# Kernel tuning notes

Hardware: AMD Instinct MI355X
Metric: run time of the kernel (lower is better)

## Reference

```python
import jax, jax.numpy as jnp
import numpy as np

B, D, OUT = 256, 63, 128
DP = D + 1  # 64


def setup_inputs() -> dict:
    key = jax.random.key(0)
    k1, k2, k3, k4, k5 = jax.random.split(key, 5)
    return {
        "x": jax.random.normal(k1, (B, D), dtype=jnp.float32),
        "protein_output": jax.random.normal(k2, (B, D), dtype=jnp.float32),
        "dynamic_output": jax.random.normal(k3, (B, D), dtype=jnp.float32),
        "W": jax.random.normal(k4, (DP ** 3, OUT), dtype=jnp.float32) * 0.02,
        "b": jax.random.normal(k5, (OUT,), dtype=jnp.float32) * 0.02,
    }


def reference(x, protein_output, dynamic_output, W, b):
    bsz = x.shape[0]
    ones = jnp.ones((bsz, 1), dtype=x.dtype)
    a = jnp.concatenate([x, ones], axis=1)               # [B, D+1]
    p = jnp.concatenate([protein_output, ones], axis=1)   # [B, D+1]
    d = jnp.concatenate([dynamic_output, ones], axis=1)   # [B, D+1]
    # rank-1 trilinear outer product, flattened row-major: idx = (i*(D+1)+j)*(D+1)+k
    ab = jnp.einsum('bi,bj->bij', a, p)                   # [B, D+1, D+1]
    abc = jnp.einsum('bij,bk->bijk', ab, d)               # [B, D+1, D+1, D+1]
    feat = abc.reshape(bsz, -1)                           # [B, (D+1)^3]
    return feat @ W + b                                   # [B, OUT]
```

## Files before the change

### kernel.cpp

```cpp
#include <hip/hip_runtime.h>
#include <hip/hip_bf16.h>

typedef __attribute__((ext_vector_type(8))) short short8v;
typedef __attribute__((ext_vector_type(4))) float floatx4;
typedef __attribute__((ext_vector_type(4))) unsigned int uint4v;

__device__ __forceinline__ unsigned int pkbf(float a, float b) {
  __hip_bfloat162 h = __float22bfloat162_rn(make_float2(a, b));
  union { __hip_bfloat162 h; unsigned int u; } c; c.h = h;
  return c.u;
}

__global__ void bias_init(const float* __restrict__ bias, float* __restrict__ out) {
  int idx = blockIdx.x * 256 + threadIdx.x;
  out[idx] = bias[idx & 127];
}

__global__ __launch_bounds__(512)
void reduce_v3(const float* __restrict__ part, const float* __restrict__ bias,
               float* __restrict__ out) {
  const int tid = threadIdx.x;
  const int o = tid & 127;
  const int qr = tid >> 7;
  const int og = blockIdx.x * 128 + o;

  const float* pp = part + (((long)(qr * 64)) << 15) + og;
  float s0 = 0.f, s1 = 0.f, s2 = 0.f, s3 = 0.f;
  #pragma unroll 4
  for (int n = 0; n < 64; n += 4) {
    s0 += __builtin_nontemporal_load(pp + ((long)n << 15));
    s1 += __builtin_nontemporal_load(pp + ((long)(n + 1) << 15));
    s2 += __builtin_nontemporal_load(pp + ((long)(n + 2) << 15));
    s3 += __builtin_nontemporal_load(pp + ((long)(n + 3) << 15));
  }
  float sum = (s0 + s1) + (s2 + s3);

  __shared__ float red[3][128];
  if (qr) red[qr - 1][o] = sum;
  __syncthreads();
  if (qr == 0)
    out[og] = sum + red[0][o] + red[1][o] + red[2][o] + bias[o];
}

__global__ __launch_bounds__(512, 2)
void tfn_gemm_v3(const float* __restrict__ X, const float* __restrict__ P,
                 const float* __restrict__ Dyn, const float* __restrict__ W,
                 float* __restrict__ part) {
  __shared__ __align__(16) float wt0[4160];
  __shared__ __align__(16) float wt1[4160];
  __shared__ float p_lds[16][256];

  const int tid = threadIdx.x;
  const int wv = tid >> 6, lane = tid & 63;
  const int q = lane >> 4, l16 = lane & 15;
  const int r = wv & 3;
  const int cg = wv >> 2;

  const int c = blockIdx.x;
  const int i = c >> 2;
  const int j0 = (c & 3) << 4;

  const uint4v* wsrc = (const uint4v*)(W + (((long)c) << 10) * 128);

  uint4v rg0 = __builtin_nontemporal_load(&wsrc[tid]);
  uint4v rg1 = __builtin_nontemporal_load(&wsrc[512 + tid]);

  for (int idx = tid; idx < 256 * 16; idx += 512) {
    int bb = idx >> 4, jj = idx & 15;
    int j = j0 + jj;
    p_lds[jj][bb] = (j < 63) ? P[bb * 63 + j] : 1.0f;
  }

  float e[4][2][8];
  #pragma unroll
  for (int rt = 0; rt < 4; ++rt) {
    int brow = (r << 6) + (rt << 4) + l16;
    float av = (i < 63) ? X[brow * 63 + i] : 1.0f;
    #pragma unroll
    for (int h = 0; h < 2; ++h) {
      int kb = (h << 5) + (q << 3);
      #pragma unroll
      for (int t = 0; t < 8; ++t) {
        int k = kb + t;
        float dv = (k < 63) ? Dyn[brow * 63 + k] : 1.0f;
        e[rt][h][t] = av * dv;
      }
    }
  }

  const int Lf0 = tid << 2;
  const int Lf1 = (tid + 512) << 2;
  const int d0 = Lf0 + ((Lf0 >> 8) << 2);
  const int d1 = Lf1 + ((Lf1 >> 8) << 2);

  *(uint4v*)&wt0[d0] = rg0;
  *(uint4v*)&wt0[d1] = rg1;
  rg0 = __builtin_nontemporal_load(&wsrc[1024 + tid]);
  rg1 = __builtin_nontemporal_load(&wsrc[1536 + tid]);

  floatx4 acc[4][4];
  #pragma unroll
  for (int a = 0; a < 4; ++a)
    #pragma unroll
    for (int b = 0; b < 4; ++b) acc[a][b] = (floatx4)0.0f;

  const int wbase = q * 1040 + (cg << 6) + l16;
  const int prow = (r << 6) + l16;

  __syncthreads();

  for (int jj = 0; jj < 16; ++jj) {
    float pb[4];
    #pragma unroll
    for (int rt = 0; rt < 4; ++rt)
      pb[rt] = p_lds[jj][prow + (rt << 4)];

    {
      *(uint4v*)&wt1[d0] = rg0;
      *(uint4v*)&wt1[d1] = rg1;
      if (jj < 15) {
        rg0 = __builtin_nontemporal_load(&wsrc[(2 * jj + 2) * 1024 + tid]);
        rg1 = __builtin_nontemporal_load(&wsrc[(2 * jj + 2) * 1024 + 512 + tid]);
      }

      float w[4][8];
      #pragma unroll
      for (int nt = 0; nt < 4; ++nt)
        #pragma unroll
        for (int t = 0; t < 8; ++t)
          w[nt][t] = wt0[wbase + (nt << 4) + t * 128 + ((t >> 1) << 2)];

      union { short8v v; unsigned int u[4]; } fb[4], fa[4];
      #pragma unroll
      for (int nt = 0; nt < 4; ++nt)
        #pragma unroll
        for (int v2 = 0; v2 < 4; ++v2)
          fb[nt].u[v2] = pkbf(w[nt][2 * v2], w[nt][2 * v2 + 1]);
      #pragma unroll
      for (int rt = 0; rt < 4; ++rt)
        #pragma unroll
        for (int v2 = 0; v2 < 4; ++v2)
          fa[rt].u[v2] = pkbf(pb[rt] * e[rt][0][2 * v2], pb[rt] * e[rt][0][2 * v2 + 1]);
      #pragma unroll
      for (int rt = 0; rt < 4; ++rt)
        #pragma unroll
        for (int nt = 0; nt < 4; ++nt)
          acc[rt][nt] = __builtin_amdgcn_mfma_f32_16x16x32_bf16(
              fa[rt].v, fb[nt].v, acc[rt][nt], 0, 0, 0);

      __syncthreads();
    }

    {
      if (jj < 15) {
        *(uint4v*)&wt0[d0] = rg0;
        *(uint4v*)&wt0[d1] = rg1;
        rg0 = __builtin_nontemporal_load(&wsrc[(2 * jj + 3) * 1024 + tid]);
        rg1 = __builtin_nontemporal_load(&wsrc[(2 * jj + 3) * 1024 + 512 + tid]);
      }

      float w[4][8];
      #pragma unroll
      for (int nt = 0; nt < 4; ++nt)
        #pragma unroll
        for (int t = 0; t < 8; ++t)
          w[nt][t] = wt1[wbase + (nt << 4) + t * 128 + ((t >> 1) << 2)];

      union { short8v v; unsigned int u[4]; } fb[4], fa[4];
      #pragma unroll
      for (int nt = 0; nt < 4; ++nt)
        #pragma unroll
        for (int v2 = 0; v2 < 4; ++v2)
          fb[nt].u[v2] = pkbf(w[nt][2 * v2], w[nt][2 * v2 + 1]);
      #pragma unroll
      for (int rt = 0; rt < 4; ++rt)
        #pragma unroll
        for (int v2 = 0; v2 < 4; ++v2)
          fa[rt].u[v2] = pkbf(pb[rt] * e[rt][1][2 * v2], pb[rt] * e[rt][1][2 * v2 + 1]);
      #pragma unroll
      for (int rt = 0; rt < 4; ++rt)
        #pragma unroll
        for (int nt = 0; nt < 4; ++nt)
          acc[rt][nt] = __builtin_amdgcn_mfma_f32_16x16x32_bf16(
              fa[rt].v, fb[nt].v, acc[rt][nt], 0, 0, 0);

      if (jj < 15) __syncthreads();
    }
  }

  float* pt = part + ((long)c << 15);
  #pragma unroll
  for (int rt = 0; rt < 4; ++rt)
    #pragma unroll
    for (int nt = 0; nt < 4; ++nt) {
      int col = (cg << 6) + (nt << 4) + l16;
      #pragma unroll
      for (int g = 0; g < 4; ++g) {
        int brow = (r << 6) + (rt << 4) + (q << 2) + g;
        pt[brow * 128 + col] = acc[rt][nt][g];
      }
    }
}

__global__ __launch_bounds__(512, 2)
void tfn_gemm(const float* __restrict__ X, const float* __restrict__ P,
              const float* __restrict__ Dyn, const float* __restrict__ W,
              float* __restrict__ out) {
  __shared__ float p_lds[16][256];

  const int tid = threadIdx.x;
  const int wv = tid >> 6, lane = tid & 63;
  const int q = lane >> 4, l16 = lane & 15;
  const int r = wv & 3;
  const int cg = wv >> 2;

  const int c = blockIdx.x;
  const int i = c >> 2;
  const int j0 = (c & 3) << 4;
  const long gk0 = (long)c << 10;

  for (int idx = tid; idx < 256 * 16; idx += 512) {
    int bb = idx >> 4, jj = idx & 15;
    int j = j0 + jj;
    p_lds[jj][bb] = (j < 63) ? P[bb * 63 + j] : 1.0f;
  }

  float e[4][2][8];
  #pragma unroll
  for (int rt = 0; rt < 4; ++rt) {
    int brow = (r << 6) + (rt << 4) + l16;
    float av = (i < 63) ? X[brow * 63 + i] : 1.0f;
    #pragma unroll
    for (int h = 0; h < 2; ++h) {
      int kb = (h << 5) + (q << 3);
      #pragma unroll
      for (int t = 0; t < 8; ++t) {
        int k = kb + t;
        float dv = (k < 63) ? Dyn[brow * 63 + k] : 1.0f;
        e[rt][h][t] = av * dv;
      }
    }
  }

  floatx4 acc[4][4];
  #pragma unroll
  for (int a = 0; a < 4; ++a)
    #pragma unroll
    for (int b = 0; b < 4; ++b) acc[a][b] = (floatx4)0.0f;

  __syncthreads();

  const float* wstep = W + (gk0 + (q << 3)) * 128 + (cg << 6) + l16;

  float wA[4][8], wB[4][8];
  #pragma unroll
  for (int nt = 0; nt < 4; ++nt)
    #pragma unroll
    for (int t = 0; t < 8; ++t)
      wA[nt][t] = wstep[t * 128 + nt * 16];

  for (int jj = 0; jj < 16; ++jj) {
    float pb[4];
    #pragma unroll
    for (int rt = 0; rt < 4; ++rt)
      pb[rt] = p_lds[jj][(r << 6) + (rt << 4) + l16];

    {
      const float* wp = wstep + ((long)(2 * jj + 1) << 12);
      #pragma unroll
      for (int nt = 0; nt < 4; ++nt)
        #pragma unroll
        for (int t = 0; t < 8; ++t)
          wB[nt][t] = wp[t * 128 + nt * 16];

      union { short8v v; unsigned int u[4]; } fb[4], fa[4];
      #pragma unroll
      for (int nt = 0; nt < 4; ++nt)
        #pragma unroll
        for (int v2 = 0; v2 < 4; ++v2)
          fb[nt].u[v2] = pkbf(wA[nt][2 * v2], wA[nt][2 * v2 + 1]);
      #pragma unroll
      for (int rt = 0; rt < 4; ++rt)
        #pragma unroll
        for (int v2 = 0; v2 < 4; ++v2)
          fa[rt].u[v2] = pkbf(pb[rt] * e[rt][0][2 * v2], pb[rt] * e[rt][0][2 * v2 + 1]);
      #pragma unroll
      for (int rt = 0; rt < 4; ++rt)
        #pragma unroll
        for (int nt = 0; nt < 4; ++nt)
          acc[rt][nt] = __builtin_amdgcn_mfma_f32_16x16x32_bf16(
              fa[rt].v, fb[nt].v, acc[rt][nt], 0, 0, 0);
    }

    {
      if (jj < 15) {
        const float* wp = wstep + ((long)(2 * jj + 2) << 12);
        #pragma unroll
        for (int nt = 0; nt < 4; ++nt)
          #pragma unroll
          for (int t = 0; t < 8; ++t)
            wA[nt][t] = wp[t * 128 + nt * 16];
      }

      union { short8v v; unsigned int u[4]; } fb[4], fa[4];
      #pragma unroll
      for (int nt = 0; nt < 4; ++nt)
        #pragma unroll
        for (int v2 = 0; v2 < 4; ++v2)
          fb[nt].u[v2] = pkbf(wB[nt][2 * v2], wB[nt][2 * v2 + 1]);
      #pragma unroll
      for (int rt = 0; rt < 4; ++rt)
        #pragma unroll
        for (int v2 = 0; v2 < 4; ++v2)
          fa[rt].u[v2] = pkbf(pb[rt] * e[rt][1][2 * v2], pb[rt] * e[rt][1][2 * v2 + 1]);
      #pragma unroll
      for (int rt = 0; rt < 4; ++rt)
        #pragma unroll
        for (int nt = 0; nt < 4; ++nt)
          acc[rt][nt] = __builtin_amdgcn_mfma_f32_16x16x32_bf16(
              fa[rt].v, fb[nt].v, acc[rt][nt], 0, 0, 0);
    }
  }

  #pragma unroll
  for (int rt = 0; rt < 4; ++rt)
    #pragma unroll
    for (int nt = 0; nt < 4; ++nt) {
      int col = (cg << 6) + (nt << 4) + l16;
      #pragma unroll
      for (int g = 0; g < 4; ++g) {
        int brow = (r << 6) + (rt << 4) + (q << 2) + g;
        atomicAdd(&out[brow * 128 + col], acc[rt][nt][g]);
      }
    }
}

extern "C" void kernel_launch(void* const* d_in, const int* in_sizes, int n_in,
                              void* d_out, int out_size, void* d_ws, size_t ws_size,
                              hipStream_t stream) {
  const float* x   = (const float*)d_in[0];
  const float* p   = (const float*)d_in[1];
  const float* dyn = (const float*)d_in[2];
  const float* W   = (const float*)d_in[3];
  const float* b   = (const float*)d_in[4];
  float* out = (float*)d_out;

  const size_t part_bytes = (size_t)256 * 32768 * sizeof(float);

  if (d_ws != nullptr && ws_size >= part_bytes) {
    float* part = (float*)d_ws;
    tfn_gemm_v3<<<256, 512, 0, stream>>>(x, p, dyn, W, part);
    reduce_v3<<<256, 512, 0, stream>>>(part, b, out);
  } else {
    bias_init<<<128, 256, 0, stream>>>(b, out);
    tfn_gemm<<<256, 512, 0, stream>>>(x, p, dyn, W, out);
  }
}
```

Before: 226.5 us.

## Split GEMM by output column quarters to shrink partial buffer and reduction

The work split changes from (i, j-quarter) blocks covering all 128 outputs to (i, 32-column quarter) blocks that loop over all 64 j values. Each block now writes a 256x32 partial, so the partial workspace and the reduce kernel's reads shrink from 64 to 16 partials per output. P is staged into LDS in full (64x257, padded), and the W tile is double-buffered in padded LDS rows. Each wave now does fewer MFMAs per barrier and synchronizes 64 times instead of 32, which raises barrier overhead relative to compute.

```diff
diff --git a/kernel.cpp b/kernel.cpp
--- a/kernel.cpp
+++ b/kernel.cpp
@@ -3,7 +3,6 @@
 
 typedef __attribute__((ext_vector_type(8))) short short8v;
 typedef __attribute__((ext_vector_type(4))) float floatx4;
-typedef __attribute__((ext_vector_type(4))) unsigned int uint4v;
 
 __device__ __forceinline__ unsigned int pkbf(float a, float b) {
   __hip_bfloat162 h = __float22bfloat162_rn(make_float2(a, b));
@@ -17,65 +16,68 @@
 }
 
 __global__ __launch_bounds__(512)
-void reduce_v3(const float* __restrict__ part, const float* __restrict__ bias,
+void reduce_v5(const float* __restrict__ part, const float* __restrict__ bias,
                float* __restrict__ out) {
   const int tid = threadIdx.x;
-  const int o = tid & 127;
+  const int col = tid & 127;
   const int qr = tid >> 7;
-  const int og = blockIdx.x * 128 + o;
-
-  const float* pp = part + (((long)(qr * 64)) << 15) + og;
+  const int b = blockIdx.x;
+
+  const float* pp = part + (long)qr * 16 * 32768 + (long)(col >> 5) * 8192
+                    + b * 32 + (col & 31);
   float s0 = 0.f, s1 = 0.f, s2 = 0.f, s3 = 0.f;
-  #pragma unroll 4
-  for (int n = 0; n < 64; n += 4) {
-    s0 += __builtin_nontemporal_load(pp + ((long)n << 15));
-    s1 += __builtin_nontemporal_load(pp + ((long)(n + 1) << 15));
-    s2 += __builtin_nontemporal_load(pp + ((long)(n + 2) << 15));
-    s3 += __builtin_nontemporal_load(pp + ((long)(n + 3) << 15));
+  #pragma unroll
+  for (int n = 0; n < 16; n += 4) {
+    s0 += __builtin_nontemporal_load(pp + (long)n * 32768);
+    s1 += __builtin_nontemporal_load(pp + (long)(n + 1) * 32768);
+    s2 += __builtin_nontemporal_load(pp + (long)(n + 2) * 32768);
+    s3 += __builtin_nontemporal_load(pp + (long)(n + 3) * 32768);
   }
   float sum = (s0 + s1) + (s2 + s3);
 
   __shared__ float red[3][128];
-  if (qr) red[qr - 1][o] = sum;
+  if (qr) red[qr - 1][col] = sum;
   __syncthreads();
   if (qr == 0)
-    out[og] = sum + red[0][o] + red[1][o] + red[2][o] + bias[o];
+    out[b * 128 + col] = sum + red[0][col] + red[1][col] + red[2][col] + bias[col];
 }
 
 __global__ __launch_bounds__(512, 2)
-void tfn_gemm_v3(const float* __restrict__ X, const float* __restrict__ P,
+void tfn_gemm_v5(const float* __restrict__ X, const float* __restrict__ P,
                  const float* __restrict__ Dyn, const float* __restrict__ W,
                  float* __restrict__ part) {
-  __shared__ __align__(16) float wt0[4160];
-  __shared__ __align__(16) float wt1[4160];
-  __shared__ float p_lds[16][256];
+  __shared__ __align__(16) float wt[2][64 * 33];
+  __shared__ float p_lds[64][257];
 
   const int tid = threadIdx.x;
   const int wv = tid >> 6, lane = tid & 63;
   const int q = lane >> 4, l16 = lane & 15;
-  const int r = wv & 3;
-  const int cg = wv >> 2;
-
-  const int c = blockIdx.x;
-  const int i = c >> 2;
-  const int j0 = (c & 3) << 4;
-
-  const uint4v* wsrc = (const uint4v*)(W + (((long)c) << 10) * 128);
-
-  uint4v rg0 = __builtin_nontemporal_load(&wsrc[tid]);
-  uint4v rg1 = __builtin_nontemporal_load(&wsrc[512 + tid]);
-
-  for (int idx = tid; idx < 256 * 16; idx += 512) {
-    int bb = idx >> 4, jj = idx & 15;
-    int j = j0 + jj;
-    p_lds[jj][bb] = (j < 63) ? P[bb * 63 + j] : 1.0f;
-  }
-
-  float e[4][2][8];
-  #pragma unroll
-  for (int rt = 0; rt < 4; ++rt) {
-    int brow = (r << 6) + (rt << 4) + l16;
-    float av = (i < 63) ? X[brow * 63 + i] : 1.0f;
+
+  const int bx = blockIdx.x;
+  const int ig = bx >> 2;
+  const int cq = bx & 3;
+
+  const int lrow = tid >> 3, lc4 = tid & 7;
+  const float* wsrc = W + ((long)ig << 19) + (cq << 5) + lrow * 128 + (lc4 << 2);
+
+  floatx4 rg = __builtin_nontemporal_load((const floatx4*)wsrc);
+
+  #pragma unroll 4
+  for (int k = 0; k < 32; ++k) {
+    int idx = tid + (k << 9);
+    if (idx < 16128) {
+      int bb = idx / 63;
+      int jj = idx - bb * 63;
+      p_lds[jj][bb] = P[idx];
+    }
+  }
+  if (tid < 256) p_lds[63][tid] = 1.0f;
+
+  float e[2][2][8];
+  #pragma unroll
+  for (int rt = 0; rt < 2; ++rt) {
+    int brow = (wv << 5) + (rt << 4) + l16;
+    float av = (ig < 63) ? X[brow * 63 + ig] : 1.0f;
     #pragma unroll
     for (int h = 0; h < 2; ++h) {
       int kb = (h << 5) + (q << 3);
@@ -88,116 +90,77 @@
     }
   }
 
-  const int Lf0 = tid << 2;
-  const int Lf1 = (tid + 512) << 2;
-  const int d0 = Lf0 + ((Lf0 >> 8) << 2);
-  const int d1 = Lf1 + ((Lf1 >> 8) << 2);
-
-  *(uint4v*)&wt0[d0] = rg0;
-  *(uint4v*)&wt0[d1] = rg1;
-  rg0 = __builtin_nontemporal_load(&wsrc[1024 + tid]);
-  rg1 = __builtin_nontemporal_load(&wsrc[1536 + tid]);
-
-  floatx4 acc[4][4];
-  #pragma unroll
-  for (int a = 0; a < 4; ++a)
-    #pragma unroll
-    for (int b = 0; b < 4; ++b) acc[a][b] = (floatx4)0.0f;
-
-  const int wbase = q * 1040 + (cg << 6) + l16;
-  const int prow = (r << 6) + l16;
+  floatx4 acc[2][2];
+  #pragma unroll
+  for (int a = 0; a < 2; ++a)
+    #pragma unroll
+    for (int b = 0; b < 2; ++b) acc[a][b] = (floatx4)0.0f;
+
+  {
+    float* wd = &wt[0][lrow * 33 + (lc4 << 2)];
+    wd[0] = rg.x; wd[1] = rg.y; wd[2] = rg.z; wd[3] = rg.w;
+  }
+  rg = __builtin_nontemporal_load((const floatx4*)(wsrc + (1 << 13)));
+
+  const int wrb = (q << 3) * 33 + l16;
+  const int prow = (wv << 5) + l16;
 
   __syncthreads();
 
-  for (int jj = 0; jj < 16; ++jj) {
-    float pb[4];
-    #pragma unroll
-    for (int rt = 0; rt < 4; ++rt)
-      pb[rt] = p_lds[jj][prow + (rt << 4)];
-
-    {
-      *(uint4v*)&wt1[d0] = rg0;
-      *(uint4v*)&wt1[d1] = rg1;
-      if (jj < 15) {
-        rg0 = __builtin_nontemporal_load(&wsrc[(2 * jj + 2) * 1024 + tid]);
-        rg1 = __builtin_nontemporal_load(&wsrc[(2 * jj + 2) * 1024 + 512 + tid]);
-      }
-
-      float w[4][8];
-      #pragma unroll
-      for (int nt = 0; nt < 4; ++nt)
+  for (int j = 0; j < 64; ++j) {
+    float pbv[2];
+    pbv[0] = p_lds[j][prow];
+    pbv[1] = p_lds[j][prow + 16];
+
+    if (j < 63) {
+      float* wd = &wt[(j + 1) & 1][lrow * 33 + (lc4 << 2)];
+      wd[0] = rg.x; wd[1] = rg.y; wd[2] = rg.z; wd[3] = rg.w;
+      if (j < 62)
+        rg = __builtin_nontemporal_load((const floatx4*)(wsrc + ((long)(j + 2) << 13)));
+    }
+
+    const float* wcur = wt[j & 1];
+    #pragma unroll
+    for (int h = 0; h < 2; ++h) {
+      float w[2][8];
+      #pragma unroll
+      for (int nt = 0; nt < 2; ++nt)
         #pragma unroll
         for (int t = 0; t < 8; ++t)
-          w[nt][t] = wt0[wbase + (nt << 4) + t * 128 + ((t >> 1) << 2)];
-
-      union { short8v v; unsigned int u[4]; } fb[4], fa[4];
-      #pragma unroll
-      for (int nt = 0; nt < 4; ++nt)
+          w[nt][t] = wcur[wrb + h * 1056 + t * 33 + (nt << 4)];
+
+      union { short8v v; unsigned int u[4]; } fb[2], fa[2];
+      #pragma unroll
+      for (int nt = 0; nt < 2; ++nt)
         #pragma unroll
         for (int v2 = 0; v2 < 4; ++v2)
           fb[nt].u[v2] = pkbf(w[nt][2 * v2], w[nt][2 * v2 + 1]);
       #pragma unroll
-      for (int rt = 0; rt < 4; ++rt)
-        #pragma unroll
-        for (int v2 = 0; v2 < 4; ++v2)
-          fa[rt].u[v2] = pkbf(pb[rt] * e[rt][0][2 * v2], pb[rt] * e[rt][0][2 * v2 + 1]);
-      #pragma unroll
-      for (int rt = 0; rt < 4; ++rt)
-        #pragma unroll
-        for (int nt = 0; nt < 4; ++nt)
+      for (int rt = 0; rt < 2; ++rt)
+        #pragma unroll
+        for (int v2 = 0; v2 < 4; ++v2)
+          fa[rt].u[v2] = pkbf(pbv[rt] * e[rt][h][2 * v2],
+                              pbv[rt] * e[rt][h][2 * v2 + 1]);
+      #pragma unroll
+      for (int rt = 0; rt < 2; ++rt)
+        #pragma unroll
+        for (int nt = 0; nt < 2; ++nt)
           acc[rt][nt] = __builtin_amdgcn_mfma_f32_16x16x32_bf16(
               fa[rt].v, fb[nt].v, acc[rt][nt], 0, 0, 0);
-
-      __syncthreads();
-    }
-
-    {
-      if (jj < 15) {
-        *(uint4v*)&wt0[d0] = rg0;
-        *(uint4v*)&wt0[d1] = rg1;
-        rg0 = __builtin_nontemporal_load(&wsrc[(2 * jj + 3) * 1024 + tid]);
-        rg1 = __builtin_nontemporal_load(&wsrc[(2 * jj + 3) * 1024 + 512 + tid]);
-      }
-
-      float w[4][8];
-      #pragma unroll
-      for (int nt = 0; nt < 4; ++nt)
-        #pragma unroll
-        for (int t = 0; t < 8; ++t)
-          w[nt][t] = wt1[wbase + (nt << 4) + t * 128 + ((t >> 1) << 2)];
-
-      union { short8v v; unsigned int u[4]; } fb[4], fa[4];
-      #pragma unroll
-      for (int nt = 0; nt < 4; ++nt)
-        #pragma unroll
-        for (int v2 = 0; v2 < 4; ++v2)
-          fb[nt].u[v2] = pkbf(w[nt][2 * v2], w[nt][2 * v2 + 1]);
-      #pragma unroll
-      for (int rt = 0; rt < 4; ++rt)
-        #pragma unroll
-        for (int v2 = 0; v2 < 4; ++v2)
-          fa[rt].u[v2] = pkbf(pb[rt] * e[rt][1][2 * v2], pb[rt] * e[rt][1][2 * v2 + 1]);
-      #pragma unroll
-      for (int rt = 0; rt < 4; ++rt)
-        #pragma unroll
-        for (int nt = 0; nt < 4; ++nt)
-          acc[rt][nt] = __builtin_amdgcn_mfma_f32_16x16x32_bf16(
-              fa[rt].v, fb[nt].v, acc[rt][nt], 0, 0, 0);
-
-      if (jj < 15) __syncthreads();
-    }
-  }
-
-  float* pt = part + ((long)c << 15);
-  #pragma unroll
-  for (int rt = 0; rt < 4; ++rt)
-    #pragma unroll
-    for (int nt = 0; nt < 4; ++nt) {
-      int col = (cg << 6) + (nt << 4) + l16;
+    }
+    __syncthreads();
+  }
+
+  float* pt = part + ((long)bx << 13);
+  #pragma unroll
+  for (int rt = 0; rt < 2; ++rt)
+    #pragma unroll
+    for (int nt = 0; nt < 2; ++nt) {
+      int cl = (nt << 4) + l16;
       #pragma unroll
       for (int g = 0; g < 4; ++g) {
-        int brow = (r << 6) + (rt << 4) + (q << 2) + g;
-        pt[brow * 128 + col] = acc[rt][nt][g];
+        int row = (wv << 5) + (rt << 4) + (q << 2) + g;
+        pt[row * 32 + cl] = acc[rt][nt][g];
       }
     }
 }
@@ -345,12 +308,12 @@
   const float* b   = (const float*)d_in[4];
   float* out = (float*)d_out;
 
-  const size_t part_bytes = (size_t)256 * 32768 * sizeof(float);
+  const size_t part_bytes = (size_t)256 * 8192 * sizeof(float);
 
   if (d_ws != nullptr && ws_size >= part_bytes) {
     float* part = (float*)d_ws;
-    tfn_gemm_v3<<<256, 512, 0, stream>>>(x, p, dyn, W, part);
-    reduce_v3<<<256, 512, 0, stream>>>(part, b, out);
+    tfn_gemm_v5<<<256, 512, 0, stream>>>(x, p, dyn, W, part);
+    reduce_v5<<<256, 512, 0, stream>>>(part, b, out);
   } else {
     bias_init<<<128, 256, 0, stream>>>(b, out);
     tfn_gemm<<<256, 512, 0, stream>>>(x, p, dyn, W, out);
```

Result: slower. 237.4 us (+4.8%).
